# Performance work log

Measured on AMD Instinct MI355X. Metric: run time of the kernel, lower is better.

The kernel has to match this reference:

```python
import jax, jax.numpy as jnp
import numpy as np

HEADS, DH = 8, 64
DIM = HEADS * DH
ONION, SC = 15, 4
N_VELO, N_SURF = 28504, 3682
N = N_VELO + N_SURF
SURF_KEEP = 3586  # = 16 + (N_SURF - 112)
FIRST_LAP = 500
NT = (ONION + 1) * SC  # 64 tokens
SCALE = DH ** -0.5
EPS = 1e-5


def _attend(tok, Wq, Wk, Wv):
    # tok: [B,H,T,D]
    q, k, v = tok @ Wq, tok @ Wk, tok @ Wv
    a = jax.nn.softmax(jnp.einsum('bhqd,bhkd->bhqk', q, k) * SCALE, axis=-1)
    return jnp.einsum('bhqk,bhkd->bhqd', a, v)


def setup_inputs() -> dict:
    rng = np.random.default_rng(0)
    perm = rng.permutation(N)
    surf_idx = jnp.asarray(np.sort(perm[:N_SURF]), jnp.int32)
    velo_idx = jnp.asarray(np.sort(perm[N_SURF:]), jnp.int32)
    # onion layer labels: first 500 velo points are lap 0 (exactly 500 ones in row 0)
    onion_lab = np.concatenate([np.zeros(FIRST_LAP, np.int64),
                                rng.integers(1, ONION, N_VELO - FIRST_LAP)])
    onion_index = jnp.asarray((onion_lab[None] == np.arange(ONION)[:, None]).astype(np.float32))
    first_lap_idx = jnp.arange(FIRST_LAP, dtype=jnp.int32)
    closest_idx = jnp.asarray(rng.integers(0, SURF_KEEP, N_VELO), jnp.int32)
    labels = jnp.asarray(rng.integers(0, SC, SURF_KEEP), jnp.int32)
    ks = iter(jax.random.split(jax.random.key(0), 32))
    p = lambda shape: jax.random.normal(next(ks), shape, jnp.float32) * 0.02
    z = lambda n: jnp.zeros((n,), jnp.float32)
    x = jax.random.normal(next(ks), (1, N, DIM), jnp.float32)
    return dict(
        x=x, onion_index=onion_index,
        W_fx=p((DIM, DIM)), b_fx=z(DIM),
        W_x=p((DIM, DIM)), b_x=z(DIM),
        Wq1=p((DH, DH)), Wk1=p((DH, DH)), Wv1=p((DH, DH)),
        Wq=p((DH, DH)), Wk=p((DH, DH)), Wv=p((DH, DH)),
        gamma=jnp.ones((NT,), jnp.float32), beta=z(NT),
        W_ws=p((DIM, SC)), b_ws=z(SC),
        W_vv=p((DIM, ONION * SC)), b_vv=z(ONION * SC),
        W_vc=p((DIM, ONION * SC)), b_vc=z(ONION * SC),
        W_out=p((DIM, DIM)), b_out=z(DIM),
        surf_idx=surf_idx, velo_idx=velo_idx, first_lap_idx=first_lap_idx,
        closest_idx=closest_idx, labels=labels)


def reference(x, onion_index, W_fx, b_fx, W_x, b_x, Wq1, Wk1, Wv1, Wq, Wk, Wv,
              gamma, beta, W_ws, b_ws, W_vv, b_vv, W_vc, b_vc, W_out, b_out,
              surf_idx, velo_idx, first_lap_idx, closest_idx, labels):
    B = x.shape[0]
    fx = x @ W_fx + b_fx                                   # in_project_fx
    surf_fx = fx[:, surf_idx]                              # [B,N_SURF,DIM]
    velo_fx = fx[:, velo_idx]                              # [B,N_VELO,DIM]
    # ---- coarse attention: first onion lap + all surface points ----
    fl = velo_fx[:, first_lap_idx]                         # [B,500,DIM]
    tok1 = jnp.concatenate([fl, surf_fx], axis=1)
    tok1 = tok1.reshape(B, -1, HEADS, DH).transpose(0, 2, 1, 3)
    out1 = _attend(tok1, Wq1, Wk1, Wv1)
    velo_first_lap = out1[:, :, :FIRST_LAP].transpose(0, 2, 1, 3).reshape(B, FIRST_LAP, DIM)
    surf_first_lap = out1[:, :, FIRST_LAP:].transpose(0, 2, 1, 3).reshape(B, N_SURF, DIM)
    # ---- fine attention: cluster-mask mean pooling expressed as segment-mean einsum ----
    velo_cluster = labels[closest_idx]                     # [N_VELO]
    onehot_v = (velo_cluster[None] == jnp.arange(SC)[:, None]).astype(fx.dtype)   # [SC,N_VELO]
    # == torch: (velo_fx * onion_mask * cluster_mask).mean(over all N_VELO points)
    new_velo_tokens = jnp.einsum('lp,cp,bpd->blcd', onion_index, onehot_v, velo_fx) / N_VELO
    new_velo_tokens = new_velo_tokens.reshape(B, ONION * SC, DIM)
    surf_keep = jnp.concatenate([surf_fx[:, :16], surf_fx[:, 112:]], axis=1)      # [B,3586,DIM]
    onehot_s = (labels[None] == jnp.arange(SC)[:, None]).astype(fx.dtype)
    surf_tokens = jnp.einsum('cp,bpd->bcd', onehot_s, surf_keep) / SURF_KEEP
    tokens = jnp.concatenate([surf_tokens, new_velo_tokens], axis=1)              # [B,NT,DIM]
    # LayerNorm over the TOKEN axis (torch permutes to [B,DIM,NT] then LayerNorm(NT))
    t = tokens.transpose(0, 2, 1)
    mu = t.mean(-1, keepdims=True)
    var = ((t - mu) ** 2).mean(-1, keepdims=True)
    tokens = ((t - mu) / jnp.sqrt(var + EPS) * gamma + beta).transpose(0, 2, 1)
    tok = tokens.reshape(B, NT, HEADS, DH).transpose(0, 2, 1, 3)
    out_tok = _attend(tok, Wq, Wk, Wv)                     # [B,H,NT,DH]
    # ---- T2P ----
    xm = x @ W_x + b_x                                     # in_project_x
    surf_x = xm[:, surf_idx]
    velo_x = xm[:, velo_idx]
    out_surf = out_tok[:, :, :SC].reshape(B, SC, DIM)      # raw row-major reshape, as in torch
    feat_surf = (surf_x @ W_ws + b_ws) @ out_surf
    out_velo = out_tok[:, :, SC:].transpose(0, 2, 1, 3).reshape(B, ONION * SC, DIM)
    feat_velo = (velo_x @ W_vv + b_vv) @ out_velo
    feat_velo_car = (surf_x @ W_vc + b_vc) @ out_velo
    feat_surf = (feat_surf + feat_velo_car) / 2.0 + surf_first_lap
    feat_velo = feat_velo.at[:, first_lap_idx].add(velo_first_lap)
    new_feature = jnp.zeros_like(x)
    new_feature = new_feature.at[:, surf_idx].set(feat_surf)
    new_feature = new_feature.at[:, velo_idx].set(feat_velo)
    return new_feature @ W_out + b_out                     # to_out
```

## Files before the change

kernel.cpp:

```cpp
#include <hip/hip_runtime.h>

#define N_TOT 32186
#define NV    28504
#define NS    3682
#define DIM   512
#define HEADS 8
#define DH    64
#define FL    500
#define NQ1   4182
#define NQP   4224
#define SK    3586
#define NTOK  64
#define ONION 15
#define SC    4
#define SCALE 0.125f
#define EPS   1e-5f

typedef unsigned short u16;
typedef __bf16 bf16x8 __attribute__((ext_vector_type(8)));
typedef float  f32x4  __attribute__((ext_vector_type(4)));

static __device__ inline void bsplit(float f, u16& hi, u16& lo) {
    __bf16 h = (__bf16)f;
    __bf16 l = (__bf16)(f - (float)h);
    hi = __builtin_bit_cast(u16, h);
    lo = __builtin_bit_cast(u16, l);
}
static __device__ inline uint2 pk2(const u16* s) {
    uint2 w;
    w.x = (unsigned)s[0] | ((unsigned)s[1] << 16);
    w.y = (unsigned)s[2] | ((unsigned)s[3] << 16);
    return w;
}

__global__ __launch_bounds__(256) void k_dual_mm(const float* __restrict__ A,
    const float* __restrict__ W1, const float* __restrict__ b1,
    const float* __restrict__ W2, const float* __restrict__ b2,
    float* __restrict__ C1, float* __restrict__ C2, int M)
{
    __shared__ __align__(16) float As[16][64];
    __shared__ __align__(16) float B1s[16][64];
    __shared__ __align__(16) float B2s[16][64];
    const int tid = threadIdx.x;
    const int bm = blockIdx.x * 64, bn = blockIdx.y * 64;
    const int tx = tid & 15, ty = tid >> 4;
    const int lr = tid >> 2, lc = (tid & 3) << 2;
    const int ar = bm + lr;
    float acc1[4][4] = {}, acc2[4][4] = {};
    for (int k0 = 0; k0 < 512; k0 += 16) {
        float4 av = {0,0,0,0};
        if (ar < M) av = *(const float4*)(A + (size_t)ar*512 + k0 + lc);
        As[lc+0][lr]=av.x; As[lc+1][lr]=av.y; As[lc+2][lr]=av.z; As[lc+3][lr]=av.w;
        const int wr = tid >> 4, wc = (tid & 15) << 2;
        *(float4*)&B1s[wr][wc] = *(const float4*)(W1 + (size_t)(k0+wr)*512 + bn + wc);
        *(float4*)&B2s[wr][wc] = *(const float4*)(W2 + (size_t)(k0+wr)*512 + bn + wc);
        __syncthreads();
        #pragma unroll
        for (int kk = 0; kk < 16; ++kk) {
            float4 a = *(const float4*)&As[kk][ty<<2];
            float4 u = *(const float4*)&B1s[kk][tx<<2];
            float4 v = *(const float4*)&B2s[kk][tx<<2];
            const float aa[4] = {a.x,a.y,a.z,a.w};
            const float uu[4] = {u.x,u.y,u.z,u.w};
            const float vv[4] = {v.x,v.y,v.z,v.w};
            #pragma unroll
            for (int i = 0; i < 4; ++i)
                #pragma unroll
                for (int j = 0; j < 4; ++j) {
                    acc1[i][j] = fmaf(aa[i], uu[j], acc1[i][j]);
                    acc2[i][j] = fmaf(aa[i], vv[j], acc2[i][j]);
                }
        }
        __syncthreads();
    }
    float4 bb1 = *(const float4*)(b1 + bn + (tx<<2));
    float4 bb2 = *(const float4*)(b2 + bn + (tx<<2));
    const float b1a[4] = {bb1.x,bb1.y,bb1.z,bb1.w};
    const float b2a[4] = {bb2.x,bb2.y,bb2.z,bb2.w};
    #pragma unroll
    for (int i = 0; i < 4; ++i) {
        int r = bm + (ty<<2) + i;
        if (r >= M) continue;
        float4 o1 = {acc1[i][0]+b1a[0], acc1[i][1]+b1a[1], acc1[i][2]+b1a[2], acc1[i][3]+b1a[3]};
        float4 o2 = {acc2[i][0]+b2a[0], acc2[i][1]+b2a[1], acc2[i][2]+b2a[2], acc2[i][3]+b2a[3]};
        *(float4*)(C1 + (size_t)r*512 + bn + (tx<<2)) = o1;
        *(float4*)(C2 + (size_t)r*512 + bn + (tx<<2)) = o2;
    }
}

__global__ __launch_bounds__(256) void k_mm_out(const float* __restrict__ A,
    const float* __restrict__ W, const float* __restrict__ b,
    float* __restrict__ C, int M)
{
    __shared__ __align__(16) float As[16][64];
    __shared__ __align__(16) float Bs[16][64];
    const int tid = threadIdx.x;
    const int bm = blockIdx.x * 64, bn = blockIdx.y * 64;
    const int tx = tid & 15, ty = tid >> 4;
    const int lr = tid >> 2, lc = (tid & 3) << 2;
    const int ar = bm + lr;
    float acc[4][4] = {};
    for (int k0 = 0; k0 < 512; k0 += 16) {
        float4 av = {0,0,0,0};
        if (ar < M) av = *(const float4*)(A + (size_t)ar*512 + k0 + lc);
        As[lc+0][lr]=av.x; As[lc+1][lr]=av.y; As[lc+2][lr]=av.z; As[lc+3][lr]=av.w;
        const int wr = tid >> 4, wc = (tid & 15) << 2;
        *(float4*)&Bs[wr][wc] = *(const float4*)(W + (size_t)(k0+wr)*512 + bn + wc);
        __syncthreads();
        #pragma unroll
        for (int kk = 0; kk < 16; ++kk) {
            float4 a = *(const float4*)&As[kk][ty<<2];
            float4 u = *(const float4*)&Bs[kk][tx<<2];
            const float aa[4] = {a.x,a.y,a.z,a.w};
            const float uu[4] = {u.x,u.y,u.z,u.w};
            #pragma unroll
            for (int i = 0; i < 4; ++i)
                #pragma unroll
                for (int j = 0; j < 4; ++j)
                    acc[i][j] = fmaf(aa[i], uu[j], acc[i][j]);
        }
        __syncthreads();
    }
    float4 bb = *(const float4*)(b + bn + (tx<<2));
    const float ba[4] = {bb.x,bb.y,bb.z,bb.w};
    #pragma unroll
    for (int i = 0; i < 4; ++i) {
        int r = bm + (ty<<2) + i;
        if (r >= M) continue;
        float4 o = {acc[i][0]+ba[0], acc[i][1]+ba[1], acc[i][2]+ba[2], acc[i][3]+ba[3]};
        *(float4*)(C + (size_t)r*512 + bn + (tx<<2)) = o;
    }
}

__global__ __launch_bounds__(256) void k_qkv1(const float* __restrict__ fx,
    const int* __restrict__ surf_idx, const int* __restrict__ velo_idx,
    const int* __restrict__ first_lap,
    const float* __restrict__ Wq, const float* __restrict__ Wk, const float* __restrict__ Wv,
    u16* __restrict__ Qhi, u16* __restrict__ Qlo,
    u16* __restrict__ Khi, u16* __restrict__ Klo,
    u16* __restrict__ Vthi, u16* __restrict__ Vtlo)
{
    __shared__ __align__(16) float As[16][64];
    __shared__ __align__(16) float Bs[3][16][64];
    const int tid = threadIdx.x;
    const int h = blockIdx.y;
    const int r0 = blockIdx.x * 64;
    const int tx = tid & 15, ty = tid >> 4;
    const int lr = tid >> 2, lc = (tid & 3) << 2;
    const int rr = r0 + lr;
    long src = -1;
    if (rr < NQ1) src = (rr < FL) ? velo_idx[first_lap[rr]] : surf_idx[rr - FL];
    float acc[3][4][4] = {};
    for (int k0 = 0; k0 < 64; k0 += 16) {
        float4 av = {0,0,0,0};
        if (src >= 0) av = *(const float4*)(fx + (size_t)src*512 + h*64 + k0 + lc);
        As[lc+0][lr]=av.x; As[lc+1][lr]=av.y; As[lc+2][lr]=av.z; As[lc+3][lr]=av.w;
        const int wr = tid >> 4, wc = (tid & 15) << 2;
        *(float4*)&Bs[0][wr][wc] = *(const float4*)(Wq + (k0+wr)*64 + wc);
        *(float4*)&Bs[1][wr][wc] = *(const float4*)(Wk + (k0+wr)*64 + wc);
        *(float4*)&Bs[2][wr][wc] = *(const float4*)(Wv + (k0+wr)*64 + wc);
        __syncthreads();
        #pragma unroll
        for (int kk = 0; kk < 16; ++kk) {
            float4 a = *(const float4*)&As[kk][ty<<2];
            const float aa[4] = {a.x,a.y,a.z,a.w};
            #pragma unroll
            for (int mm = 0; mm < 3; ++mm) {
                float4 bv = *(const float4*)&Bs[mm][kk][tx<<2];
                const float bb[4] = {bv.x,bv.y,bv.z,bv.w};
                #pragma unroll
                for (int i = 0; i < 4; ++i)
                    #pragma unroll
                    for (int j = 0; j < 4; ++j)
                        acc[mm][i][j] = fmaf(aa[i], bb[j], acc[mm][i][j]);
            }
        }
        __syncthreads();
    }
    #pragma unroll
    for (int i = 0; i < 4; ++i) {
        int r = r0 + (ty<<2) + i;
        size_t qb = ((size_t)h*NQP + r)*64 + (tx<<2);
        u16 qh_[4], ql_[4], kh_[4], kl_[4];
        #pragma unroll
        for (int j = 0; j < 4; ++j) {
            bsplit(acc[0][i][j]*SCALE, qh_[j], ql_[j]);
            bsplit(acc[1][i][j],       kh_[j], kl_[j]);
        }
        *(uint2*)(Qhi + qb) = pk2(qh_);
        *(uint2*)(Qlo + qb) = pk2(ql_);
        *(uint2*)(Khi + qb) = pk2(kh_);
        *(uint2*)(Klo + qb) = pk2(kl_);
        #pragma unroll
        for (int j = 0; j < 4; ++j) {
            u16 vh_, vl_;
            bsplit(acc[2][i][j], vh_, vl_);
            size_t vb = ((size_t)h*64 + (tx<<2) + j)*NQP + r;
            Vthi[vb] = vh_;
            Vtlo[vb] = vl_;
        }
    }
}

__global__ __launch_bounds__(320) void k_attn1(
    const u16* __restrict__ Qhi, const u16* __restrict__ Qlo,
    const u16* __restrict__ Khi, const u16* __restrict__ Klo,
    const u16* __restrict__ Vthi, const u16* __restrict__ Vtlo,
    float* __restrict__ O)
{
    __shared__ __align__(16) u16 Ksh[64][72];
    __shared__ __align__(16) u16 Ksl[64][72];
    __shared__ __align__(16) u16 Vsh[64][72];
    __shared__ __align__(16) u16 Vsl[64][72];
    __shared__ __align__(16) float Ps[5][32*68];

    const int tid = threadIdx.x;
    const int wave = tid >> 6;
    const int lane = tid & 63;
    const int m = lane & 15, quad = lane >> 4;
    const int h = blockIdx.y;
    const int q0 = blockIdx.x*160 + wave*32;

    const u16* Kgh = Khi + (size_t)h*NQP*64;
    const u16* Kgl = Klo + (size_t)h*NQP*64;
    const u16* Vgh = Vthi + (size_t)h*64*NQP;
    const u16* Vgl = Vtlo + (size_t)h*64*NQP;

    bf16x8 qh[2][2], ql[2][2];
    #pragma unroll
    for (int t = 0; t < 2; ++t)
        #pragma unroll
        for (int ks = 0; ks < 2; ++ks) {
            int q = q0 + t*16 + m;
            if (q < NQP) {
                size_t off = ((size_t)h*NQP + q)*64 + ks*32 + quad*8;
                qh[t][ks] = *(const bf16x8*)(Qhi + off);
                ql[t][ks] = *(const bf16x8*)(Qlo + off);
            } else {
                #pragma unroll
                for (int j = 0; j < 8; ++j) { qh[t][ks][j] = (__bf16)0.f; ql[t][ks][j] = (__bf16)0.f; }
            }
        }

    const int sr = tid >> 2;
    const int sc = (tid & 3) << 4;
    uint4 pre[8];
    if (tid < 256) {
        size_t kb = (size_t)sr*64 + sc;
        pre[0] = *(const uint4*)(Kgh + kb);     pre[1] = *(const uint4*)(Kgh + kb + 8);
        pre[2] = *(const uint4*)(Kgl + kb);     pre[3] = *(const uint4*)(Kgl + kb + 8);
        size_t vb = (size_t)sr*NQP + sc;
        pre[4] = *(const uint4*)(Vgh + vb);     pre[5] = *(const uint4*)(Vgh + vb + 8);
        pre[6] = *(const uint4*)(Vgl + vb);     pre[7] = *(const uint4*)(Vgl + vb + 8);
    }

    f32x4 Oc[2][4];
    float mrun[2][4], lrun[2][4];
    #pragma unroll
    for (int t = 0; t < 2; ++t)
        #pragma unroll
        for (int r = 0; r < 4; ++r) {
            mrun[t][r] = -1e30f; lrun[t][r] = 0.f;
            #pragma unroll
            for (int dt = 0; dt < 4; ++dt) Oc[t][dt][r] = 0.f;
        }
    float* Pw = &Ps[wave][0];

    for (int k0 = 0; k0 < NQ1; k0 += 64) {
        __syncthreads();
        if (tid < 256) {
            *(uint4*)&Ksh[sr][sc] = pre[0];  *(uint4*)&Ksh[sr][sc+8] = pre[1];
            *(uint4*)&Ksl[sr][sc] = pre[2];  *(uint4*)&Ksl[sr][sc+8] = pre[3];
            *(uint4*)&Vsh[sr][sc] = pre[4];  *(uint4*)&Vsh[sr][sc+8] = pre[5];
            *(uint4*)&Vsl[sr][sc] = pre[6];  *(uint4*)&Vsl[sr][sc+8] = pre[7];
        }
        __syncthreads();
        const int kn = k0 + 64;
        if (kn < NQ1 && tid < 256) {
            size_t kb = ((size_t)kn + sr)*64 + sc;
            pre[0] = *(const uint4*)(Kgh + kb);     pre[1] = *(const uint4*)(Kgh + kb + 8);
            pre[2] = *(const uint4*)(Kgl + kb);     pre[3] = *(const uint4*)(Kgl + kb + 8);
            size_t vb = (size_t)sr*NQP + kn + sc;
            pre[4] = *(const uint4*)(Vgh + vb);     pre[5] = *(const uint4*)(Vgh + vb + 8);
            pre[6] = *(const uint4*)(Vgl + vb);     pre[7] = *(const uint4*)(Vgl + vb + 8);
        }

        f32x4 S[2][4];
        #pragma unroll
        for (int t = 0; t < 2; ++t)
            #pragma unroll
            for (int n = 0; n < 4; ++n)
                #pragma unroll
                for (int r = 0; r < 4; ++r) S[t][n][r] = 0.f;
        #pragma unroll
        for (int ks = 0; ks < 2; ++ks) {
            bf16x8 kh[4], kl[4];
            #pragma unroll
            for (int n = 0; n < 4; ++n) {
                kh[n] = *(const bf16x8*)&Ksh[n*16 + m][ks*32 + quad*8];
                kl[n] = *(const bf16x8*)&Ksl[n*16 + m][ks*32 + quad*8];
            }
            #pragma unroll
            for (int t = 0; t < 2; ++t)
                #pragma unroll
                for (int n = 0; n < 4; ++n)
                    S[t][n] = __builtin_amdgcn_mfma_f32_16x16x32_bf16(qh[t][ks], kh[n], S[t][n], 0,0,0);
            #pragma unroll
            for (int t = 0; t < 2; ++t)
                #pragma unroll
                for (int n = 0; n < 4; ++n)
                    S[t][n] = __builtin_amdgcn_mfma_f32_16x16x32_bf16(qh[t][ks], kl[n], S[t][n], 0,0,0);
            #pragma unroll
            for (int t = 0; t < 2; ++t)
                #pragma unroll
                for (int n = 0; n < 4; ++n)
                    S[t][n] = __builtin_amdgcn_mfma_f32_16x16x32_bf16(ql[t][ks], kh[n], S[t][n], 0,0,0);
        }
        if (kn > NQ1) {
            #pragma unroll
            for (int n = 0; n < 4; ++n)
                if (k0 + n*16 + m >= NQ1) {
                    #pragma unroll
                    for (int t = 0; t < 2; ++t)
                        #pragma unroll
                        for (int r = 0; r < 4; ++r) S[t][n][r] = -1e30f;
                }
        }

        float alpha[2][4];
        #pragma unroll
        for (int t = 0; t < 2; ++t) {
            float sm[4];
            #pragma unroll
            for (int r = 0; r < 4; ++r) {
                float v = fmaxf(fmaxf(S[t][0][r], S[t][1][r]), fmaxf(S[t][2][r], S[t][3][r]));
                v = fmaxf(v, __shfl_xor(v, 1));
                v = fmaxf(v, __shfl_xor(v, 2));
                v = fmaxf(v, __shfl_xor(v, 4));
                v = fmaxf(v, __shfl_xor(v, 8));
                float mn = fmaxf(mrun[t][r], v);
                alpha[t][r] = __expf(mrun[t][r] - mn);
                mrun[t][r] = mn;
                sm[r] = 0.f;
            }
            #pragma unroll
            for (int n = 0; n < 4; ++n)
                #pragma unroll
                for (int r = 0; r < 4; ++r) {
                    float p = __expf(S[t][n][r] - mrun[t][r]);
                    S[t][n][r] = p;
                    sm[r] += p;
                }
            #pragma unroll
            for (int r = 0; r < 4; ++r) {
                float v = sm[r];
                v += __shfl_xor(v, 1);
                v += __shfl_xor(v, 2);
                v += __shfl_xor(v, 4);
                v += __shfl_xor(v, 8);
                lrun[t][r] = lrun[t][r]*alpha[t][r] + v;
            }
        }
        #pragma unroll
        for (int t = 0; t < 2; ++t)
            #pragma unroll
            for (int dt = 0; dt < 4; ++dt)
                #pragma unroll
                for (int r = 0; r < 4; ++r) Oc[t][dt][r] *= alpha[t][r];

        #pragma unroll
        for (int t = 0; t < 2; ++t)
            #pragma unroll
            for (int n = 0; n < 4; ++n)
                #pragma unroll
                for (int r = 0; r < 4; ++r)
                    Pw[(t*16 + quad*4 + r)*68 + n*16 + m] = S[t][n][r];

        #pragma unroll
        for (int ks = 0; ks < 2; ++ks) {
            bf16x8 ah[2], al[2];
            #pragma unroll
            for (int t = 0; t < 2; ++t) {
                const float* pp = Pw + (t*16 + m)*68 + ks*32 + quad*8;
                float4 xa = *(const float4*)pp;
                float4 xb = *(const float4*)(pp + 4);
                float e0[8] = {xa.x, xa.y, xa.z, xa.w, xb.x, xb.y, xb.z, xb.w};
                #pragma unroll
                for (int j = 0; j < 8; ++j) {
                    __bf16 hb = (__bf16)e0[j];
                    ah[t][j] = hb;
                    al[t][j] = (__bf16)(e0[j] - (float)hb);
                }
            }
            bf16x8 vh[4], vl[4];
            #pragma unroll
            for (int dt = 0; dt < 4; ++dt) {
                vh[dt] = *(const bf16x8*)&Vsh[dt*16 + m][ks*32 + quad*8];
                vl[dt] = *(const bf16x8*)&Vsl[dt*16 + m][ks*32 + quad*8];
            }
            #pragma unroll
            for (int t = 0; t < 2; ++t)
                #pragma unroll
                for (int dt = 0; dt < 4; ++dt)
                    Oc[t][dt] = __builtin_amdgcn_mfma_f32_16x16x32_bf16(ah[t], vh[dt], Oc[t][dt], 0,0,0);
            #pragma unroll
            for (int t = 0; t < 2; ++t)
                #pragma unroll
                for (int dt = 0; dt < 4; ++dt)
                    Oc[t][dt] = __builtin_amdgcn_mfma_f32_16x16x32_bf16(ah[t], vl[dt], Oc[t][dt], 0,0,0);
            #pragma unroll
            for (int t = 0; t < 2; ++t)
                #pragma unroll
                for (int dt = 0; dt < 4; ++dt)
                    Oc[t][dt] = __builtin_amdgcn_mfma_f32_16x16x32_bf16(al[t], vh[dt], Oc[t][dt], 0,0,0);
        }
    }

    #pragma unroll
    for (int t = 0; t < 2; ++t) {
        float il[4];
        #pragma unroll
        for (int r = 0; r < 4; ++r) il[r] = 1.f / lrun[t][r];
        #pragma unroll
        for (int dt = 0; dt < 4; ++dt)
            #pragma unroll
            for (int r = 0; r < 4; ++r) {
                int q = q0 + t*16 + quad*4 + r;
                if (q < NQ1)
                    O[((size_t)h*NQ1 + q)*64 + dt*16 + m] = Oc[t][dt][r] * il[r];
            }
    }
}

__global__ void k_bucket_prep(const int* __restrict__ labels, const int* __restrict__ closest,
    const int* __restrict__ surf_idx, const int* __restrict__ velo_idx,
    const float* __restrict__ onion, int* __restrict__ tok_of, int* __restrict__ src_of)
{
    int r = blockIdx.x*256 + threadIdx.x;
    if (r < SK) {
        tok_of[r] = labels[r];
        int s = (r < 16) ? r : r + 96;
        src_of[r] = surf_idx[s];
    } else if (r < SK + NV) {
        int p = r - SK;
        int cl = labels[closest[p]];
        int l = 0;
        #pragma unroll
        for (int q = 1; q < ONION; ++q)
            if (onion[(size_t)q*NV + p] != 0.f) l = q;
        tok_of[r] = SC + l*SC + cl;
        src_of[r] = velo_idx[p];
    }
}

__global__ __launch_bounds__(256) void k_tokens_accum(const float* __restrict__ fx,
    const int* __restrict__ tok_of, const int* __restrict__ src_of, float* __restrict__ part)
{
    __shared__ float acc[64][256];
    const int tid = threadIdx.x;
    for (int i = tid; i < 64*256; i += 256) ((float*)acc)[i] = 0.f;
    __syncthreads();
    const int d0 = blockIdx.x << 8;
    const int R = SK + NV;
    const int per = (R + gridDim.y - 1) / gridDim.y;
    int rs = blockIdx.y * per;
    int re = rs + per; if (re > R) re = R;
    const float wS = 1.f / SK, wV = 1.f / NV;
    int r = rs;
    for (; r + 4 <= re; r += 4) {
        int t0 = tok_of[r], t1 = tok_of[r+1], t2 = tok_of[r+2], t3 = tok_of[r+3];
        int s0 = src_of[r], s1 = src_of[r+1], s2 = src_of[r+2], s3 = src_of[r+3];
        float v0 = fx[(size_t)s0*512 + d0 + tid] * ((r   < SK) ? wS : wV);
        float v1 = fx[(size_t)s1*512 + d0 + tid] * ((r+1 < SK) ? wS : wV);
        float v2 = fx[(size_t)s2*512 + d0 + tid] * ((r+2 < SK) ? wS : wV);
        float v3 = fx[(size_t)s3*512 + d0 + tid] * ((r+3 < SK) ? wS : wV);
        acc[t0][tid] += v0; acc[t1][tid] += v1; acc[t2][tid] += v2; acc[t3][tid] += v3;
    }
    for (; r < re; ++r) {
        float v = fx[(size_t)src_of[r]*512 + d0 + tid] * ((r < SK) ? wS : wV);
        acc[tok_of[r]][tid] += v;
    }
    __syncthreads();
    float* dst = part + ((size_t)blockIdx.x*gridDim.y + blockIdx.y)*64*256;
    for (int i = tid; i < 64*256; i += 256) dst[i] = acc[i >> 8][i & 255];
}

__global__ void k_tokens_reduce(const float* __restrict__ part, float* __restrict__ tokens)
{
    int idx = blockIdx.x*256 + threadIdx.x;
    int t = idx >> 9;
    int dg = idx & 511;
    int cc = dg >> 8, d = dg & 255;
    float s = 0.f;
    for (int ch = 0; ch < 64; ++ch)
        s += part[(((size_t)cc*64 + ch)*64 + t)*256 + d];
    tokens[idx] = s;
}

__global__ void k_ln(const float* __restrict__ tokens, const float* __restrict__ gamma,
    const float* __restrict__ beta, float* __restrict__ tln)
{
    int ch = blockIdx.x*256 + threadIdx.x;
    if (ch >= 512) return;
    float vals[64];
    float mu = 0.f;
    #pragma unroll
    for (int t = 0; t < 64; ++t) { vals[t] = tokens[t*512 + ch]; mu += vals[t]; }
    mu *= (1.f/64.f);
    float var = 0.f;
    #pragma unroll
    for (int t = 0; t < 64; ++t) { float d = vals[t]-mu; var = fmaf(d, d, var); }
    var *= (1.f/64.f);
    float rstd = rsqrtf(var + EPS);
    #pragma unroll
    for (int t = 0; t < 64; ++t)
        tln[t*512 + ch] = (vals[t]-mu)*rstd*gamma[t] + beta[t];
}

__global__ __launch_bounds__(256) void k_qkv2(const float* __restrict__ tln,
    const float* __restrict__ Wq, const float* __restrict__ Wk, const float* __restrict__ Wv,
    float* __restrict__ q2, float* __restrict__ k2, float* __restrict__ v2)
{
    __shared__ float Ts[64][64];
    __shared__ float Wt[3][64][65];
    const int h = blockIdx.x, tid = threadIdx.x;
    for (int i = tid; i < 4096; i += 256) {
        int t = i >> 6, d = i & 63;
        Ts[t][d] = tln[t*512 + h*64 + d];
    }
    for (int i = tid; i < 4096; i += 256) {
        int d = i >> 6, e = i & 63;
        Wt[0][e][d] = Wq[i]; Wt[1][e][d] = Wk[i]; Wt[2][e][d] = Wv[i];
    }
    __syncthreads();
    for (int o = tid; o < 4096; o += 256) {
        int t = o >> 6, e = o & 63;
        float s0 = 0.f, s1 = 0.f, s2 = 0.f;
        for (int d = 0; d < 64; ++d) {
            float xv = Ts[t][d];
            s0 = fmaf(xv, Wt[0][e][d], s0);
            s1 = fmaf(xv, Wt[1][e][d], s1);
            s2 = fmaf(xv, Wt[2][e][d], s2);
        }
        size_t idx = (size_t)h*4096 + o;
        q2[idx] = s0; k2[idx] = s1; v2[idx] = s2;
    }
}

__global__ __launch_bounds__(256) void k_attn2(const float* __restrict__ q2,
    const float* __restrict__ k2, const float* __restrict__ v2, float* __restrict__ ot)
{
    __shared__ float Qs[64][65], Ks[64][65], Vs[64][65], Ps2[64][65];
    const int h = blockIdx.x, tid = threadIdx.x;
    const float* qh = q2 + (size_t)h*4096;
    const float* kh = k2 + (size_t)h*4096;
    const float* vh = v2 + (size_t)h*4096;
    for (int i = tid; i < 4096; i += 256) {
        int t = i >> 6, e = i & 63;
        Qs[t][e] = qh[i]; Ks[t][e] = kh[i]; Vs[t][e] = vh[i];
    }
    __syncthreads();
    for (int o = tid; o < 4096; o += 256) {
        int t = o >> 6, j = o & 63;
        float s = 0.f;
        for (int e = 0; e < 64; ++e) s = fmaf(Qs[t][e], Ks[j][e], s);
        Ps2[t][j] = s * SCALE;
    }
    __syncthreads();
    if (tid < 64) {
        float mx = -1e30f;
        for (int j = 0; j < 64; ++j) mx = fmaxf(mx, Ps2[tid][j]);
        float sum = 0.f;
        for (int j = 0; j < 64; ++j) { float p = __expf(Ps2[tid][j]-mx); Ps2[tid][j] = p; sum += p; }
        float inv = 1.f / sum;
        for (int j = 0; j < 64; ++j) Ps2[tid][j] *= inv;
    }
    __syncthreads();
    for (int o = tid; o < 4096; o += 256) {
        int t = o >> 6, e = o & 63;
        float s = 0.f;
        for (int j = 0; j < 64; ++j) s = fmaf(Ps2[t][j], Vs[j][e], s);
        ot[(size_t)h*4096 + o] = s;
    }
}

__global__ void k_build_ov(const float* __restrict__ ot, float* __restrict__ osurf,
    float* __restrict__ ovelo)
{
    int i = blockIdx.x*256 + threadIdx.x;
    if (i < 2048) {
        osurf[i] = ot[((i >> 8) << 12) + (i & 255)];
    }
    int g = i - 2048;
    if (g >= 0 && g < 60*512) {
        int j = g >> 9, cch = g & 511;
        int hh = cch >> 6, d = cch & 63;
        ovelo[g] = ot[(size_t)hh*4096 + (SC + j)*64 + d];
    }
}

__global__ __launch_bounds__(256) void k_coef_surf(const float* __restrict__ xm,
    const int* __restrict__ surf_idx,
    const float* __restrict__ W_ws, const float* __restrict__ b_ws,
    const float* __restrict__ W_vc, const float* __restrict__ b_vc,
    float* __restrict__ cs, float* __restrict__ cc)
{
    __shared__ __align__(16) float As[16][516];
    __shared__ float Ws[128][64];
    const int tid = threadIdx.x;
    const int s0 = blockIdx.x * 16;
    for (int i = tid; i < 16*128; i += 256) {
        int r = i >> 7, c4 = (i & 127) << 2;
        float4 a = {0,0,0,0};
        int s = s0 + r;
        if (s < NS) a = *(const float4*)(xm + (size_t)surf_idx[s]*512 + c4);
        *(float4*)&As[r][c4] = a;
    }
    const int c = tid & 63, rg = tid >> 6;
    float acc[4] = {0,0,0,0};
    for (int k0 = 0; k0 < 512; k0 += 128) {
        __syncthreads();
        for (int i = tid; i < 128*64; i += 256) {
            int kk = i >> 6, cw = i & 63;
            int k = k0 + kk;
            Ws[kk][cw] = (cw < 4) ? W_ws[k*4 + cw] : W_vc[k*60 + (cw-4)];
        }
        __syncthreads();
        #pragma unroll 8
        for (int kk = 0; kk < 128; kk += 4) {
            float w0 = Ws[kk][c], w1 = Ws[kk+1][c], w2 = Ws[kk+2][c], w3 = Ws[kk+3][c];
            #pragma unroll
            for (int u = 0; u < 4; ++u) {
                float4 a = *(const float4*)&As[rg + (u<<2)][k0 + kk];
                acc[u] = fmaf(a.x,w0, fmaf(a.y,w1, fmaf(a.z,w2, fmaf(a.w,w3, acc[u]))));
            }
        }
    }
    #pragma unroll
    for (int u = 0; u < 4; ++u) {
        int s = s0 + rg + (u<<2);
        if (s >= NS) continue;
        if (c < 4) cs[(size_t)s*4 + c] = acc[u] + b_ws[c];
        else cc[(size_t)s*60 + (c-4)] = acc[u] + b_vc[c-4];
    }
}

__global__ __launch_bounds__(256) void k_coef_velo(const float* __restrict__ xm,
    const int* __restrict__ velo_idx, const float* __restrict__ W,
    const float* __restrict__ b, float* __restrict__ cv)
{
    __shared__ __align__(16) float As[16][516];
    __shared__ float Ws[128][64];
    const int tid = threadIdx.x;
    const int v0 = blockIdx.x * 16;
    for (int i = tid; i < 16*128; i += 256) {
        int r = i >> 7, c4 = (i & 127) << 2;
        float4 a = {0,0,0,0};
        int v = v0 + r;
        if (v < NV) a = *(const float4*)(xm + (size_t)velo_idx[v]*512 + c4);
        *(float4*)&As[r][c4] = a;
    }
    const int c = tid & 63, rg = tid >> 6;
    float acc[4] = {0,0,0,0};
    for (int k0 = 0; k0 < 512; k0 += 128) {
        __syncthreads();
        for (int i = tid; i < 128*64; i += 256) {
            int kk = i >> 6, cw = i & 63;
            Ws[kk][cw] = (cw < 60) ? W[(size_t)(k0+kk)*60 + cw] : 0.f;
        }
        __syncthreads();
        #pragma unroll 8
        for (int kk = 0; kk < 128; kk += 4) {
            float w0 = Ws[kk][c], w1 = Ws[kk+1][c], w2 = Ws[kk+2][c], w3 = Ws[kk+3][c];
            #pragma unroll
            for (int u = 0; u < 4; ++u) {
                float4 a = *(const float4*)&As[rg + (u<<2)][k0 + kk];
                acc[u] = fmaf(a.x,w0, fmaf(a.y,w1, fmaf(a.z,w2, fmaf(a.w,w3, acc[u]))));
            }
        }
    }
    if (c < 60) {
        float bb = b[c];
        #pragma unroll
        for (int u = 0; u < 4; ++u) {
            int v = v0 + rg + (u<<2);
            if (v < NV) cv[(size_t)v*60 + c] = acc[u] + bb;
        }
    }
}

__global__ __launch_bounds__(256) void k_feat_velo(const float* __restrict__ cv,
    const float* __restrict__ ovelo, const float* __restrict__ O1,
    const int* __restrict__ velo_idx, float* __restrict__ nf)
{
    __shared__ float Cs[16][64];
    const int tid = threadIdx.x;
    const int v0 = blockIdx.x * 16;
    for (int i = tid; i < 16*64; i += 256) {
        int r = i >> 6, j = i & 63;
        int v = v0 + r;
        Cs[r][j] = (j < 60 && v < NV) ? cv[(size_t)v*60 + j] : 0.f;
    }
    __syncthreads();
    const int c = tid, c2 = tid + 256;
    float a0[16], a1[16];
    #pragma unroll
    for (int r = 0; r < 16; ++r) { a0[r] = 0.f; a1[r] = 0.f; }
    #pragma unroll 4
    for (int j = 0; j < 60; ++j) {
        float e0 = ovelo[j*512 + c];
        float e1 = ovelo[j*512 + c2];
        #pragma unroll
        for (int r = 0; r < 16; ++r) {
            float cf = Cs[r][j];
            a0[r] = fmaf(cf, e0, a0[r]);
            a1[r] = fmaf(cf, e1, a1[r]);
        }
    }
    const int h0 = c >> 6, d0 = c & 63, h1 = c2 >> 6, d1 = c2 & 63;
    for (int r = 0; r < 16; ++r) {
        int v = v0 + r;
        if (v >= NV) break;
        float f0 = a0[r], f1 = a1[r];
        if (v < FL) {
            f0 += O1[((size_t)h0*NQ1 + v)*64 + d0];
            f1 += O1[((size_t)h1*NQ1 + v)*64 + d1];
        }
        size_t row = (size_t)velo_idx[v]*512;
        nf[row + c] = f0;
        nf[row + c2] = f1;
    }
}

__global__ __launch_bounds__(256) void k_feat_surf(const float* __restrict__ cs,
    const float* __restrict__ cc, const float* __restrict__ osurf,
    const float* __restrict__ ovelo, const float* __restrict__ O1,
    const int* __restrict__ surf_idx, float* __restrict__ nf)
{
    __shared__ float Cs[16][64];
    const int tid = threadIdx.x;
    const int s0 = blockIdx.x * 16;
    for (int i = tid; i < 16*64; i += 256) {
        int r = i >> 6, j = i & 63;
        int s = s0 + r;
        float v = 0.f;
        if (s < NS) v = (j < 4) ? cs[(size_t)s*4 + j] : cc[(size_t)s*60 + (j-4)];
        Cs[r][j] = v;
    }
    __syncthreads();
    const int c = tid, c2 = tid + 256;
    float a0[16], a1[16];
    #pragma unroll
    for (int r = 0; r < 16; ++r) { a0[r] = 0.f; a1[r] = 0.f; }
    #pragma unroll 4
    for (int j = 0; j < 64; ++j) {
        float e0 = (j < 4) ? osurf[j*512 + c]  : ovelo[(j-4)*512 + c];
        float e1 = (j < 4) ? osurf[j*512 + c2] : ovelo[(j-4)*512 + c2];
        #pragma unroll
        for (int r = 0; r < 16; ++r) {
            float cf = Cs[r][j];
            a0[r] = fmaf(cf, e0, a0[r]);
            a1[r] = fmaf(cf, e1, a1[r]);
        }
    }
    const int h0 = c >> 6, d0 = c & 63, h1 = c2 >> 6, d1 = c2 & 63;
    for (int r = 0; r < 16; ++r) {
        int s = s0 + r;
        if (s >= NS) break;
        float f0 = 0.5f*a0[r] + O1[((size_t)h0*NQ1 + FL + s)*64 + d0];
        float f1 = 0.5f*a1[r] + O1[((size_t)h1*NQ1 + FL + s)*64 + d1];
        size_t row = (size_t)surf_idx[s]*512;
        nf[row + c] = f0;
        nf[row + c2] = f1;
    }
}

extern "C" void kernel_launch(void* const* d_in, const int* in_sizes, int n_in,
                              void* d_out, int out_size, void* d_ws, size_t ws_size,
                              hipStream_t stream)
{
    const float* x       = (const float*)d_in[0];
    const float* onion   = (const float*)d_in[1];
    const float* W_fx    = (const float*)d_in[2];
    const float* b_fx    = (const float*)d_in[3];
    const float* W_x     = (const float*)d_in[4];
    const float* b_x     = (const float*)d_in[5];
    const float* Wq1     = (const float*)d_in[6];
    const float* Wk1     = (const float*)d_in[7];
    const float* Wv1     = (const float*)d_in[8];
    const float* Wq      = (const float*)d_in[9];
    const float* Wk      = (const float*)d_in[10];
    const float* Wv      = (const float*)d_in[11];
    const float* gamma   = (const float*)d_in[12];
    const float* beta    = (const float*)d_in[13];
    const float* W_ws    = (const float*)d_in[14];
    const float* b_ws    = (const float*)d_in[15];
    const float* W_vv    = (const float*)d_in[16];
    const float* b_vv    = (const float*)d_in[17];
    const float* W_vc    = (const float*)d_in[18];
    const float* b_vc    = (const float*)d_in[19];
    const float* W_out   = (const float*)d_in[20];
    const float* b_out   = (const float*)d_in[21];
    const int* surf_idx  = (const int*)d_in[22];
    const int* velo_idx  = (const int*)d_in[23];
    const int* first_lap = (const int*)d_in[24];
    const int* closest   = (const int*)d_in[25];
    const int* labels    = (const int*)d_in[26];
    float* out = (float*)d_out;
    float* ws  = (float*)d_ws;

    size_t o = 0;
    float* fx   = ws + o;  o += (size_t)N_TOT*512;
    float* xm   = ws + o;  o += (size_t)N_TOT*512;
    float* O1   = ws + o;  o += (size_t)HEADS*NQ1*64;
    const size_t BFSZ = (size_t)HEADS*NQP*64/2;
    u16* Qhi = (u16*)(ws + o); o += BFSZ;
    u16* Qlo = (u16*)(ws + o); o += BFSZ;
    u16* Khi = (u16*)(ws + o); o += BFSZ;
    u16* Klo = (u16*)(ws + o); o += BFSZ;
    u16* Vthi= (u16*)(ws + o); o += BFSZ;
    u16* Vtlo= (u16*)(ws + o); o += BFSZ;
    float* tokens = ws + o; o += 64*512;
    float* tln  = ws + o;  o += 64*512;
    float* q2   = ws + o;  o += 8*64*64;
    float* k2   = ws + o;  o += 8*64*64;
    float* v2   = ws + o;  o += 8*64*64;
    float* ot   = ws + o;  o += 8*64*64;
    float* osurf= ws + o;  o += 4*512;
    float* ovelo= ws + o;  o += 60*512;
    float* cs   = ws + o;  o += (size_t)NS*4;
    float* cv   = ws + o;  o += (size_t)NV*60;
    float* cc   = ws + o;  o += (size_t)NS*60;
    int* tok_of = (int*)(ws + o); o += SK + NV;
    int* src_of = (int*)(ws + o); o += SK + NV;
    float* part = ws + o;  o += (size_t)2*64*64*256;
    float* nf = fx;

    (void)in_sizes; (void)n_in; (void)out_size; (void)ws_size; (void)b_vv;

    k_dual_mm<<<dim3(503, 8), 256, 0, stream>>>(x, W_fx, b_fx, W_x, b_x, fx, xm, N_TOT);
    k_bucket_prep<<<126, 256, 0, stream>>>(labels, closest, surf_idx, velo_idx, onion, tok_of, src_of);
    k_qkv1<<<dim3(66, 8), 256, 0, stream>>>(fx, surf_idx, velo_idx, first_lap, Wq1, Wk1, Wv1,
                                            Qhi, Qlo, Khi, Klo, Vthi, Vtlo);
    k_attn1<<<dim3(27, 8), 320, 0, stream>>>(Qhi, Qlo, Khi, Klo, Vthi, Vtlo, O1);
    k_tokens_accum<<<dim3(2, 64), 256, 0, stream>>>(fx, tok_of, src_of, part);
    k_tokens_reduce<<<128, 256, 0, stream>>>(part, tokens);
    k_ln<<<2, 256, 0, stream>>>(tokens, gamma, beta, tln);
    k_qkv2<<<8, 256, 0, stream>>>(tln, Wq, Wk, Wv, q2, k2, v2);
    k_attn2<<<8, 256, 0, stream>>>(q2, k2, v2, ot);
    k_build_ov<<<128, 256, 0, stream>>>(ot, osurf, ovelo);
    k_coef_surf<<<231, 256, 0, stream>>>(xm, surf_idx, W_ws, b_ws, W_vc, b_vc, cs, cc);
    k_coef_velo<<<1782, 256, 0, stream>>>(xm, velo_idx, W_vv, b_vv, cv);
    k_feat_velo<<<1782, 256, 0, stream>>>(cv, ovelo, O1, velo_idx, nf);
    k_feat_surf<<<231, 256, 0, stream>>>(cs, cc, osurf, ovelo, O1, surf_idx, nf);
    k_mm_out<<<dim3(503, 8), 256, 0, stream>>>(nf, W_out, b_out, out, N_TOT);
}
```

Baseline: 1.517 ms.

## Replace FP32 SIMT GEMMs with split-bf16 MFMA GEMMs for projections

Replaces the scalar FP32 dual-output and output-projection GEMMs with a matrix-core kernel. It emulates FP32 accuracy by splitting each operand into high and low bf16 parts and issuing three MFMA products per tile. A small pre-kernel transposes and splits the three 512x512 weight matrices into workspace. The fused dual GEMM becomes two separate launches, so x is read twice, and the split and transpose work runs on every call.

After: 1.304 ms. 1.16x faster.

```diff
diff --git a/kernel.cpp b/kernel.cpp
--- a/kernel.cpp
+++ b/kernel.cpp
@@ -33,103 +33,140 @@
     return w;
 }
 
-__global__ __launch_bounds__(256) void k_dual_mm(const float* __restrict__ A,
-    const float* __restrict__ W1, const float* __restrict__ b1,
-    const float* __restrict__ W2, const float* __restrict__ b2,
-    float* __restrict__ C1, float* __restrict__ C2, int M)
-{
-    __shared__ __align__(16) float As[16][64];
-    __shared__ __align__(16) float B1s[16][64];
-    __shared__ __align__(16) float B2s[16][64];
+__global__ __launch_bounds__(256) void k_split_wT(
+    const float* __restrict__ W0, const float* __restrict__ W1, const float* __restrict__ W2,
+    u16* __restrict__ h0, u16* __restrict__ l0,
+    u16* __restrict__ h1, u16* __restrict__ l1,
+    u16* __restrict__ h2, u16* __restrict__ l2)
+{
+    const float* W = (blockIdx.z == 0) ? W0 : (blockIdx.z == 1) ? W1 : W2;
+    u16* th = (blockIdx.z == 0) ? h0 : (blockIdx.z == 1) ? h1 : h2;
+    u16* tl = (blockIdx.z == 0) ? l0 : (blockIdx.z == 1) ? l1 : l2;
+    __shared__ float T[32][33];
     const int tid = threadIdx.x;
-    const int bm = blockIdx.x * 64, bn = blockIdx.y * 64;
-    const int tx = tid & 15, ty = tid >> 4;
-    const int lr = tid >> 2, lc = (tid & 3) << 2;
-    const int ar = bm + lr;
-    float acc1[4][4] = {}, acc2[4][4] = {};
-    for (int k0 = 0; k0 < 512; k0 += 16) {
-        float4 av = {0,0,0,0};
-        if (ar < M) av = *(const float4*)(A + (size_t)ar*512 + k0 + lc);
-        As[lc+0][lr]=av.x; As[lc+1][lr]=av.y; As[lc+2][lr]=av.z; As[lc+3][lr]=av.w;
-        const int wr = tid >> 4, wc = (tid & 15) << 2;
-        *(float4*)&B1s[wr][wc] = *(const float4*)(W1 + (size_t)(k0+wr)*512 + bn + wc);
-        *(float4*)&B2s[wr][wc] = *(const float4*)(W2 + (size_t)(k0+wr)*512 + bn + wc);
+    const int k0 = blockIdx.x*32, n0 = blockIdx.y*32;
+    {
+        int r = tid >> 3, c = (tid & 7) << 2;
+        *(float4*)&T[r][c] = *(const float4*)(W + (size_t)(k0+r)*512 + n0 + c);
+    }
+    __syncthreads();
+    int n = tid >> 3, kk = (tid & 7) << 2;
+    u16 hh[4], ll[4];
+    #pragma unroll
+    for (int j = 0; j < 4; ++j) bsplit(T[kk+j][n], hh[j], ll[j]);
+    *(uint2*)(th + (size_t)(n0+n)*512 + k0 + kk) = pk2(hh);
+    *(uint2*)(tl + (size_t)(n0+n)*512 + k0 + kk) = pk2(ll);
+}
+
+__global__ __launch_bounds__(256) void k_mm_bf16s(const float* __restrict__ A,
+    const u16* __restrict__ Bth, const u16* __restrict__ Btl,
+    const float* __restrict__ bias, float* __restrict__ C, int M)
+{
+    __shared__ __align__(16) u16 Ash[128][72], Asl[128][72];
+    __shared__ __align__(16) u16 Bsh[64][72],  Bsl[64][72];
+    const int tid = threadIdx.x;
+    const int wave = tid >> 6, lane = tid & 63;
+    const int m = lane & 15, quad = lane >> 4;
+    const int bn = blockIdx.x * 64;
+    const int bm = blockIdx.y * 128;
+    const int wm = wave * 32;
+
+    const int ar = tid >> 1;
+    const int ac = (tid & 1) << 5;
+    const int br = tid >> 2;
+    const int bc = (tid & 3) << 4;
+
+    f32x4 acc[2][4];
+    #pragma unroll
+    for (int mt = 0; mt < 2; ++mt)
+        #pragma unroll
+        for (int nt = 0; nt < 4; ++nt)
+            #pragma unroll
+            for (int r = 0; r < 4; ++r) acc[mt][nt][r] = 0.f;
+
+    float4 pa[8];
+    uint4 pbh[2], pbl[2];
+    {
+        bool va = (bm + ar) < M;
+        const float* ap = A + (size_t)(bm+ar)*512 + ac;
+        #pragma unroll
+        for (int u = 0; u < 8; ++u)
+            pa[u] = va ? *(const float4*)(ap + u*4) : float4{0,0,0,0};
+        size_t bb = (size_t)(bn+br)*512 + bc;
+        pbh[0] = *(const uint4*)(Bth + bb); pbh[1] = *(const uint4*)(Bth + bb + 8);
+        pbl[0] = *(const uint4*)(Btl + bb); pbl[1] = *(const uint4*)(Btl + bb + 8);
+    }
+
+    for (int k0 = 0; k0 < 512; k0 += 64) {
         __syncthreads();
         #pragma unroll
-        for (int kk = 0; kk < 16; ++kk) {
-            float4 a = *(const float4*)&As[kk][ty<<2];
-            float4 u = *(const float4*)&B1s[kk][tx<<2];
-            float4 v = *(const float4*)&B2s[kk][tx<<2];
-            const float aa[4] = {a.x,a.y,a.z,a.w};
-            const float uu[4] = {u.x,u.y,u.z,u.w};
-            const float vv[4] = {v.x,v.y,v.z,v.w};
-            #pragma unroll
-            for (int i = 0; i < 4; ++i)
-                #pragma unroll
-                for (int j = 0; j < 4; ++j) {
-                    acc1[i][j] = fmaf(aa[i], uu[j], acc1[i][j]);
-                    acc2[i][j] = fmaf(aa[i], vv[j], acc2[i][j]);
-                }
-        }
+        for (int u = 0; u < 8; ++u) {
+            u16 hh[4], ll[4];
+            bsplit(pa[u].x, hh[0], ll[0]);
+            bsplit(pa[u].y, hh[1], ll[1]);
+            bsplit(pa[u].z, hh[2], ll[2]);
+            bsplit(pa[u].w, hh[3], ll[3]);
+            *(uint2*)&Ash[ar][ac + u*4] = pk2(hh);
+            *(uint2*)&Asl[ar][ac + u*4] = pk2(ll);
+        }
+        *(uint4*)&Bsh[br][bc]   = pbh[0];  *(uint4*)&Bsh[br][bc+8] = pbh[1];
+        *(uint4*)&Bsl[br][bc]   = pbl[0];  *(uint4*)&Bsl[br][bc+8] = pbl[1];
         __syncthreads();
-    }
-    float4 bb1 = *(const float4*)(b1 + bn + (tx<<2));
-    float4 bb2 = *(const float4*)(b2 + bn + (tx<<2));
-    const float b1a[4] = {bb1.x,bb1.y,bb1.z,bb1.w};
-    const float b2a[4] = {bb2.x,bb2.y,bb2.z,bb2.w};
-    #pragma unroll
-    for (int i = 0; i < 4; ++i) {
-        int r = bm + (ty<<2) + i;
-        if (r >= M) continue;
-        float4 o1 = {acc1[i][0]+b1a[0], acc1[i][1]+b1a[1], acc1[i][2]+b1a[2], acc1[i][3]+b1a[3]};
-        float4 o2 = {acc2[i][0]+b2a[0], acc2[i][1]+b2a[1], acc2[i][2]+b2a[2], acc2[i][3]+b2a[3]};
-        *(float4*)(C1 + (size_t)r*512 + bn + (tx<<2)) = o1;
-        *(float4*)(C2 + (size_t)r*512 + bn + (tx<<2)) = o2;
-    }
-}
-
-__global__ __launch_bounds__(256) void k_mm_out(const float* __restrict__ A,
-    const float* __restrict__ W, const float* __restrict__ b,
-    float* __restrict__ C, int M)
-{
-    __shared__ __align__(16) float As[16][64];
-    __shared__ __align__(16) float Bs[16][64];
-    const int tid = threadIdx.x;
-    const int bm = blockIdx.x * 64, bn = blockIdx.y * 64;
-    const int tx = tid & 15, ty = tid >> 4;
-    const int lr = tid >> 2, lc = (tid & 3) << 2;
-    const int ar = bm + lr;
-    float acc[4][4] = {};
-    for (int k0 = 0; k0 < 512; k0 += 16) {
-        float4 av = {0,0,0,0};
-        if (ar < M) av = *(const float4*)(A + (size_t)ar*512 + k0 + lc);
-        As[lc+0][lr]=av.x; As[lc+1][lr]=av.y; As[lc+2][lr]=av.z; As[lc+3][lr]=av.w;
-        const int wr = tid >> 4, wc = (tid & 15) << 2;
-        *(float4*)&Bs[wr][wc] = *(const float4*)(W + (size_t)(k0+wr)*512 + bn + wc);
-        __syncthreads();
-        #pragma unroll
-        for (int kk = 0; kk < 16; ++kk) {
-            float4 a = *(const float4*)&As[kk][ty<<2];
-            float4 u = *(const float4*)&Bs[kk][tx<<2];
-            const float aa[4] = {a.x,a.y,a.z,a.w};
-            const float uu[4] = {u.x,u.y,u.z,u.w};
-            #pragma unroll
-            for (int i = 0; i < 4; ++i)
-                #pragma unroll
-                for (int j = 0; j < 4; ++j)
-                    acc[i][j] = fmaf(aa[i], uu[j], acc[i][j]);
-        }
-        __syncthreads();
-    }
-    float4 bb = *(const float4*)(b + bn + (tx<<2));
-    const float ba[4] = {bb.x,bb.y,bb.z,bb.w};
-    #pragma unroll
-    for (int i = 0; i < 4; ++i) {
-        int r = bm + (ty<<2) + i;
-        if (r >= M) continue;
-        float4 o = {acc[i][0]+ba[0], acc[i][1]+ba[1], acc[i][2]+ba[2], acc[i][3]+ba[3]};
-        *(float4*)(C + (size_t)r*512 + bn + (tx<<2)) = o;
-    }
+        const int kn = k0 + 64;
+        if (kn < 512) {
+            bool va = (bm + ar) < M;
+            const float* ap = A + (size_t)(bm+ar)*512 + kn + ac;
+            #pragma unroll
+            for (int u = 0; u < 8; ++u)
+                pa[u] = va ? *(const float4*)(ap + u*4) : float4{0,0,0,0};
+            size_t bb = (size_t)(bn+br)*512 + kn + bc;
+            pbh[0] = *(const uint4*)(Bth + bb); pbh[1] = *(const uint4*)(Bth + bb + 8);
+            pbl[0] = *(const uint4*)(Btl + bb); pbl[1] = *(const uint4*)(Btl + bb + 8);
+        }
+        #pragma unroll
+        for (int ks = 0; ks < 2; ++ks) {
+            bf16x8 ah[2], al[2];
+            #pragma unroll
+            for (int mt = 0; mt < 2; ++mt) {
+                ah[mt] = *(const bf16x8*)&Ash[wm + mt*16 + m][ks*32 + quad*8];
+                al[mt] = *(const bf16x8*)&Asl[wm + mt*16 + m][ks*32 + quad*8];
+            }
+            bf16x8 bh[4], bl[4];
+            #pragma unroll
+            for (int nt = 0; nt < 4; ++nt) {
+                bh[nt] = *(const bf16x8*)&Bsh[nt*16 + m][ks*32 + quad*8];
+                bl[nt] = *(const bf16x8*)&Bsl[nt*16 + m][ks*32 + quad*8];
+            }
+            #pragma unroll
+            for (int mt = 0; mt < 2; ++mt)
+                #pragma unroll
+                for (int nt = 0; nt < 4; ++nt)
+                    acc[mt][nt] = __builtin_amdgcn_mfma_f32_16x16x32_bf16(ah[mt], bh[nt], acc[mt][nt], 0,0,0);
+            #pragma unroll
+            for (int mt = 0; mt < 2; ++mt)
+                #pragma unroll
+                for (int nt = 0; nt < 4; ++nt)
+                    acc[mt][nt] = __builtin_amdgcn_mfma_f32_16x16x32_bf16(ah[mt], bl[nt], acc[mt][nt], 0,0,0);
+            #pragma unroll
+            for (int mt = 0; mt < 2; ++mt)
+                #pragma unroll
+                for (int nt = 0; nt < 4; ++nt)
+                    acc[mt][nt] = __builtin_amdgcn_mfma_f32_16x16x32_bf16(al[mt], bh[nt], acc[mt][nt], 0,0,0);
+        }
+    }
+
+    #pragma unroll
+    for (int mt = 0; mt < 2; ++mt)
+        #pragma unroll
+        for (int nt = 0; nt < 4; ++nt) {
+            float bsv = bias[bn + nt*16 + m];
+            #pragma unroll
+            for (int r = 0; r < 4; ++r) {
+                int row = bm + wm + mt*16 + quad*4 + r;
+                if (row < M)
+                    C[(size_t)row*512 + bn + nt*16 + m] = acc[mt][nt][r] + bsv;
+            }
+        }
 }
 
 __global__ __launch_bounds__(256) void k_qkv1(const float* __restrict__ fx,
@@ -820,6 +857,13 @@
     u16* Klo = (u16*)(ws + o); o += BFSZ;
     u16* Vthi= (u16*)(ws + o); o += BFSZ;
     u16* Vtlo= (u16*)(ws + o); o += BFSZ;
+    const size_t WSPL = (size_t)512*512/2;
+    u16* Wfxh = (u16*)(ws + o); o += WSPL;
+    u16* Wfxl = (u16*)(ws + o); o += WSPL;
+    u16* Wxh  = (u16*)(ws + o); o += WSPL;
+    u16* Wxl  = (u16*)(ws + o); o += WSPL;
+    u16* Woh  = (u16*)(ws + o); o += WSPL;
+    u16* Wol  = (u16*)(ws + o); o += WSPL;
     float* tokens = ws + o; o += 64*512;
     float* tln  = ws + o;  o += 64*512;
     float* q2   = ws + o;  o += 8*64*64;
@@ -836,9 +880,12 @@
     float* part = ws + o;  o += (size_t)2*64*64*256;
     float* nf = fx;
 
-    (void)in_sizes; (void)n_in; (void)out_size; (void)ws_size; (void)b_vv;
-
-    k_dual_mm<<<dim3(503, 8), 256, 0, stream>>>(x, W_fx, b_fx, W_x, b_x, fx, xm, N_TOT);
+    (void)in_sizes; (void)n_in; (void)out_size; (void)ws_size;
+
+    k_split_wT<<<dim3(16,16,3), 256, 0, stream>>>(W_fx, W_x, W_out,
+                                                  Wfxh, Wfxl, Wxh, Wxl, Woh, Wol);
+    k_mm_bf16s<<<dim3(8, 252), 256, 0, stream>>>(x, Wfxh, Wfxl, b_fx, fx, N_TOT);
+    k_mm_bf16s<<<dim3(8, 252), 256, 0, stream>>>(x, Wxh,  Wxl,  b_x,  xm, N_TOT);
     k_bucket_prep<<<126, 256, 0, stream>>>(labels, closest, surf_idx, velo_idx, onion, tok_of, src_of);
     k_qkv1<<<dim3(66, 8), 256, 0, stream>>>(fx, surf_idx, velo_idx, first_lap, Wq1, Wk1, Wv1,
                                             Qhi, Qlo, Khi, Klo, Vthi, Vtlo);
@@ -853,5 +900,5 @@
     k_coef_velo<<<1782, 256, 0, stream>>>(xm, velo_idx, W_vv, b_vv, cv);
     k_feat_velo<<<1782, 256, 0, stream>>>(cv, ovelo, O1, velo_idx, nf);
     k_feat_surf<<<231, 256, 0, stream>>>(cs, cc, osurf, ovelo, O1, surf_idx, nf);
-    k_mm_out<<<dim3(503, 8), 256, 0, stream>>>(nf, W_out, b_out, out, N_TOT);
-}
+    k_mm_bf16s<<<dim3(8, 252), 256, 0, stream>>>(nf, Woh, Wol, b_out, out, N_TOT);
+}
```
